# Optimization experiments

Hardware: AMD Instinct MI355X
Metric: run time of the kernel (lower is better)

The kernel has to match this reference:

```python
import jax, jax.numpy as jnp
import numpy as np

B, T, C = 4096, 64, 64

def setup_inputs() -> dict:
    key = jax.random.key(0)
    ks = jax.random.split(key, 6)
    x = jax.random.normal(ks[0], (B, T, C), dtype=jnp.float32)
    # torch Linear stores weight as [out, in]; kaiming-uniform-ish scale ~ 1/sqrt(C)
    s = 1.0 / np.sqrt(C)
    Wk = jax.random.uniform(ks[1], (C, C), jnp.float32, -s, s)
    Wq = jax.random.uniform(ks[2], (C, C), jnp.float32, -s, s)
    Wv = jax.random.uniform(ks[3], (C, C), jnp.float32, -s, s)
    Wp = jax.random.uniform(ks[4], (C, C), jnp.float32, -s, s)
    bp = jax.random.uniform(ks[5], (C,), jnp.float32, -s, s)
    return {"x": x, "Wk": Wk, "Wq": Wq, "Wv": Wv, "Wp": Wp, "bp": bp}

def reference(x, Wk, Wq, Wv, Wp, bp):
    Bc, Tc, Cc = x.shape
    k = x @ Wk.T                      # [B,T,C]
    q = x @ Wq.T
    v = x @ Wv.T
    wei = jnp.einsum('btc,bsc->bts', q, k) * (Cc ** -0.5)  # [B,T,T]
    causal = jnp.tril(jnp.ones((Tc, Tc), dtype=bool))
    wei = jnp.where(causal, wei, -jnp.inf)
    wei = jax.nn.softmax(wei, axis=-1)
    out = jnp.einsum('bts,bsc->btc', wei, v)  # [B,T,C]
    return out @ Wp.T + bp
```

## Files before the change

### kernel.cpp

```cpp
#include <hip/hip_runtime.h>
#include <hip/hip_bf16.h>


typedef __attribute__((ext_vector_type(8))) short bf16x8;
typedef __attribute__((ext_vector_type(4))) short bf16x4;
typedef __attribute__((ext_vector_type(4))) float f32x4;

#define MFMA32(a, b, c) __builtin_amdgcn_mfma_f32_16x16x32_bf16(a, b, c, 0, 0, 0)
#define LOG2E 1.44269504088896f
#define BSTR 68

__device__ __forceinline__ unsigned short f2b(float f) {
    return __builtin_bit_cast(unsigned short, __float2bfloat16(f));
}

__device__ __forceinline__ bf16x4 pack4(f32x4 a, float s) {
    bf16x4 r;
    r[0] = (short)f2b(a[0] * s); r[1] = (short)f2b(a[1] * s);
    r[2] = (short)f2b(a[2] * s); r[3] = (short)f2b(a[3] * s);
    return r;
}

__device__ __forceinline__ bf16x4 zero4() {
    bf16x4 r; r[0] = 0; r[1] = 0; r[2] = 0; r[3] = 0; return r;
}

__device__ __forceinline__ bf16x8 cat(bf16x4 lo, bf16x4 hi) {
    bf16x8 r;
    r[0] = lo[0]; r[1] = lo[1]; r[2] = lo[2]; r[3] = lo[3];
    r[4] = hi[0]; r[5] = hi[1]; r[6] = hi[2]; r[7] = hi[3];
    return r;
}

__device__ __forceinline__ bf16x8 cvt8(float4 a, float4 b) {
    bf16x8 r;
    r[0] = (short)f2b(a.x); r[1] = (short)f2b(a.y);
    r[2] = (short)f2b(a.z); r[3] = (short)f2b(a.w);
    r[4] = (short)f2b(b.x); r[5] = (short)f2b(b.y);
    r[6] = (short)f2b(b.z); r[7] = (short)f2b(b.w);
    return r;
}

__device__ __forceinline__ bf16x8 cvt8s(float4 a, float4 b, float s) {
    bf16x8 r;
    r[0] = (short)f2b(a.x * s); r[1] = (short)f2b(a.y * s);
    r[2] = (short)f2b(a.z * s); r[3] = (short)f2b(a.w * s);
    r[4] = (short)f2b(b.x * s); r[5] = (short)f2b(b.y * s);
    r[6] = (short)f2b(b.z * s); r[7] = (short)f2b(b.w * s);
    return r;
}

__device__ __forceinline__ int swz(int row, int col) {
    return row * 64 + (col ^ ((row & 7) << 3));
}

__device__ __forceinline__ void compute_batch(
    const short* __restrict__ lw, float* __restrict__ bnc, const bf16x8 xf[8],
    const float* __restrict__ bp, float* __restrict__ ob, int lane, int r, int g)
{
    const short* Wk = lw;
    const short* Wq = lw + 4096;
    const short* Wv = lw + 8192;
    const short* Wp = lw + 12288;

    bf16x8 kT8[2][4];
    #pragma unroll
    for (int cm2 = 0; cm2 < 2; ++cm2) {
        bf16x4 lo[4];
        #pragma unroll
        for (int h = 0; h < 2; ++h) {
            const int cm = cm2 * 2 + h;
            bf16x8 a0 = *(const bf16x8*)(Wk + swz(cm * 16 + r, g * 8));
            bf16x8 a1 = *(const bf16x8*)(Wk + swz(cm * 16 + r, 32 + g * 8));
            #pragma unroll
            for (int sm = 0; sm < 4; ++sm) {
                f32x4 acc = {0.f, 0.f, 0.f, 0.f};
                acc = MFMA32(a0, xf[sm * 2], acc);
                acc = MFMA32(a1, xf[sm * 2 + 1], acc);
                if (h == 0) lo[sm] = pack4(acc, 1.0f);
                else kT8[cm2][sm] = cat(lo[sm], pack4(acc, 1.0f));
            }
        }
    }

    bf16x8 q8[2][4];
    #pragma unroll
    for (int cm2 = 0; cm2 < 2; ++cm2) {
        bf16x4 lo[4];
        #pragma unroll
        for (int h = 0; h < 2; ++h) {
            const int cm = cm2 * 2 + h;
            bf16x8 a0 = *(const bf16x8*)(Wq + swz(cm * 16 + r, g * 8));
            bf16x8 a1 = *(const bf16x8*)(Wq + swz(cm * 16 + r, 32 + g * 8));
            #pragma unroll
            for (int tt = 0; tt < 4; ++tt) {
                f32x4 acc = {0.f, 0.f, 0.f, 0.f};
                acc = MFMA32(a0, xf[tt * 2], acc);
                acc = MFMA32(a1, xf[tt * 2 + 1], acc);
                if (h == 0) lo[tt] = pack4(acc, 1.0f);
                else q8[cm2][tt] = cat(lo[tt], pack4(acc, 1.0f));
            }
        }
    }

    bf16x4 P[4][4];
    #pragma unroll
    for (int tn = 0; tn < 4; ++tn) {
        f32x4 st[4];
        #pragma unroll
        for (int sm = 0; sm < 4; ++sm) {
            if (sm > tn) continue;
            f32x4 acc = {0.f, 0.f, 0.f, 0.f};
            acc = MFMA32(kT8[0][sm], q8[0][tn], acc);
            acc = MFMA32(kT8[1][sm], q8[1][tn], acc);
            st[sm] = acc;
        }
        float mx = -1e30f;
        #pragma unroll
        for (int sm = 0; sm < 4; ++sm) {
            if (sm > tn) continue;
            #pragma unroll
            for (int j = 0; j < 4; ++j) {
                float v = st[sm][j];
                if (sm == tn) v = ((g * 4 + j) <= r) ? v : -1e30f;
                st[sm][j] = v;
                mx = fmaxf(mx, v);
            }
        }
        mx = fmaxf(mx, __shfl_xor(mx, 16));
        mx = fmaxf(mx, __shfl_xor(mx, 32));
        float sum = 0.f;
        #pragma unroll
        for (int sm = 0; sm < 4; ++sm) {
            if (sm > tn) continue;
            #pragma unroll
            for (int j = 0; j < 4; ++j) {
                float e = exp2f((st[sm][j] - mx) * LOG2E);
                st[sm][j] = e;
                sum += e;
            }
        }
        sum += __shfl_xor(sum, 16);
        sum += __shfl_xor(sum, 32);
        float inv = __builtin_amdgcn_rcpf(sum);
        #pragma unroll
        for (int sm = 0; sm < 4; ++sm)
            P[sm][tn] = (sm <= tn) ? pack4(st[sm], inv) : zero4();
    }

    bf16x8 v8[4][2];
    #pragma unroll
    for (int cm = 0; cm < 4; ++cm) {
        bf16x8 b0 = *(const bf16x8*)(Wv + swz(cm * 16 + r, g * 8));
        bf16x8 b1 = *(const bf16x8*)(Wv + swz(cm * 16 + r, 32 + g * 8));
        bf16x4 tmp[4];
        #pragma unroll
        for (int tv = 0; tv < 4; ++tv) {
            f32x4 acc = {0.f, 0.f, 0.f, 0.f};
            acc = MFMA32(xf[tv * 2], b0, acc);
            acc = MFMA32(xf[tv * 2 + 1], b1, acc);
            tmp[tv] = pack4(acc, 1.0f);
        }
        v8[cm][0] = cat(tmp[0], tmp[1]);
        v8[cm][1] = cat(tmp[2], tmp[3]);
    }

    bf16x8 o28[4][2];
    #pragma unroll
    for (int tn = 0; tn < 4; ++tn) {
        bf16x8 pt80 = cat(P[0][tn], P[1][tn]);
        bf16x8 pt81 = cat(P[2][tn], P[3][tn]);
        bf16x4 c[4];
        #pragma unroll
        for (int cm = 0; cm < 4; ++cm) {
            f32x4 acc = {0.f, 0.f, 0.f, 0.f};
            acc = MFMA32(v8[cm][0], pt80, acc);
            if (tn >= 2) acc = MFMA32(v8[cm][1], pt81, acc);
            c[cm] = pack4(acc, 1.0f);
        }
        o28[tn][0] = cat(c[0], c[1]);
        o28[tn][1] = cat(c[2], c[3]);
    }

    bf16x8 wp0[4], wp1[4];
    float4 bias4[4];
    #pragma unroll
    for (int om = 0; om < 4; ++om) {
        wp0[om] = cat(*(const bf16x4*)(Wp + swz(om * 16 + r, g * 4)),
                      *(const bf16x4*)(Wp + swz(om * 16 + r, 16 + g * 4)));
        wp1[om] = cat(*(const bf16x4*)(Wp + swz(om * 16 + r, 32 + g * 4)),
                      *(const bf16x4*)(Wp + swz(om * 16 + r, 48 + g * 4)));
        bias4[om] = *(const float4*)(bp + om * 16 + g * 4);
    }
    #pragma unroll
    for (int tn = 0; tn < 4; ++tn) {
        #pragma unroll
        for (int om = 0; om < 4; ++om) {
            f32x4 acc = {0.f, 0.f, 0.f, 0.f};
            acc = MFMA32(wp0[om], o28[tn][0], acc);
            acc = MFMA32(wp1[om], o28[tn][1], acc);
            float4 o;
            o.x = acc[0] + bias4[om].x; o.y = acc[1] + bias4[om].y;
            o.z = acc[2] + bias4[om].z; o.w = acc[3] + bias4[om].w;
            *(float4*)(bnc + r * BSTR + om * 16 + g * 4) = o;
        }
        asm volatile("s_waitcnt lgkmcnt(0)" ::: "memory");
        #pragma unroll
        for (int i = 0; i < 4; ++i) {
            float4 v = *(const float4*)(bnc + (i * 4 + (lane >> 4)) * BSTR + (lane & 15) * 4);
            *(float4*)(ob + tn * 1024 + i * 256 + lane * 4) = v;
        }
        asm volatile("" ::: "memory");
    }
}

__global__ __launch_bounds__(512, 2) void attn_fused_kernel(
    const float* __restrict__ x,
    const float* __restrict__ wk,
    const float* __restrict__ wq,
    const float* __restrict__ wvw,
    const float* __restrict__ wp,
    const float* __restrict__ bp,
    float* __restrict__ out)
{
    __shared__ short lw[16384];
    __shared__ float lbounce[8 * 16 * BSTR];

    const int tid  = threadIdx.x;
    const int wv_  = tid >> 6;
    const int lane = tid & 63;
    const int r = lane & 15;
    const int g = lane >> 4;
    float* bnc = lbounce + wv_ * (16 * BSTR);
    const long b0 = (long)blockIdx.x * 8 + wv_;
    const long b1 = b0 + 2048;

    const float* xb0 = x + b0 * 4096;
    float4 raw[8][2];
    #pragma unroll
    for (int f = 0; f < 8; ++f) {
        const float* p = xb0 + ((f >> 1) * 16 + r) * 64 + (f & 1) * 32 + g * 8;
        raw[f][0] = *(const float4*)p;
        raw[f][1] = *(const float4*)(p + 4);
    }

    {
        const int row  = tid >> 1;
        const int half = tid & 1;
        const float* wsrc = (row < 64) ? wk : (row < 128) ? wq : (row < 192) ? wvw : wp;
        const float s = (row >= 64 && row < 128) ? 0.125f : 1.0f;
        const int lrow = row & 63;
        #pragma unroll
        for (int i = 0; i < 4; ++i) {
            const int grp = half * 4 + i;
            const float* p = wsrc + lrow * 64 + grp * 8;
            float4 a = *(const float4*)p;
            float4 b = *(const float4*)(p + 4);
            *(bf16x8*)(lw + row * 64 + ((grp ^ (row & 7)) * 8)) = cvt8s(a, b, s);
        }
    }

    bf16x8 xf[8];
    #pragma unroll
    for (int f = 0; f < 8; ++f)
        xf[f] = cvt8(raw[f][0], raw[f][1]);

    __syncthreads();

    const float* xb1 = x + b1 * 4096;
    float4 raw1[8][2];
    #pragma unroll
    for (int f = 0; f < 8; ++f) {
        const float* p = xb1 + ((f >> 1) * 16 + r) * 64 + (f & 1) * 32 + g * 8;
        raw1[f][0] = *(const float4*)p;
        raw1[f][1] = *(const float4*)(p + 4);
    }

    compute_batch(lw, bnc, xf, bp, out + b0 * 4096, lane, r, g);

    bf16x8 xf1[8];
    #pragma unroll
    for (int f = 0; f < 8; ++f)
        xf1[f] = cvt8(raw1[f][0], raw1[f][1]);

    compute_batch(lw, bnc, xf1, bp, out + b1 * 4096, lane, r, g);
}

extern "C" void kernel_launch(void* const* d_in, const int* in_sizes, int n_in,
                              void* d_out, int out_size, void* d_ws, size_t ws_size,
                              hipStream_t stream) {
    const float* x  = (const float*)d_in[0];
    const float* wk = (const float*)d_in[1];
    const float* wq = (const float*)d_in[2];
    const float* wv = (const float*)d_in[3];
    const float* wp = (const float*)d_in[4];
    const float* bp = (const float*)d_in[5];

    attn_fused_kernel<<<256, 512, 0, stream>>>(x, wk, wq, wv, wp, bp, (float*)d_out);
}
```

Measured before the change: 29.96 us.

## Split each batch's query tiles across a wave pair and double the grid

Each batch is now handled by two waves instead of one. One wave computes query tiles {1,2} and the other {0,3}, which balances the causal work between them. The grid doubles to 512 blocks so each CU holds more resident waves and can hide more latency. In exchange, both waves of a pair recompute the full K and V projections and load the same x rows. Each block also redoes the weight-to-LDS conversion, so total arithmetic and memory traffic grow.

```diff
diff --git a/kernel.cpp b/kernel.cpp
--- a/kernel.cpp
+++ b/kernel.cpp
@@ -54,7 +54,8 @@
     return row * 64 + (col ^ ((row & 7) << 3));
 }
 
-__device__ __forceinline__ void compute_batch(
+template<int TNA, int TNB>
+__device__ __forceinline__ void compute_half(
     const short* __restrict__ lw, float* __restrict__ bnc, const bf16x8 xf[8],
     const float* __restrict__ bp, float* __restrict__ ob, int lane, int r, int g)
 {
@@ -83,36 +84,38 @@
         }
     }
 
-    bf16x8 q8[2][4];
+    bf16x8 q8[2][2];
     #pragma unroll
     for (int cm2 = 0; cm2 < 2; ++cm2) {
-        bf16x4 lo[4];
+        bf16x4 lo[2];
         #pragma unroll
         for (int h = 0; h < 2; ++h) {
             const int cm = cm2 * 2 + h;
             bf16x8 a0 = *(const bf16x8*)(Wq + swz(cm * 16 + r, g * 8));
             bf16x8 a1 = *(const bf16x8*)(Wq + swz(cm * 16 + r, 32 + g * 8));
             #pragma unroll
-            for (int tt = 0; tt < 4; ++tt) {
+            for (int ti = 0; ti < 2; ++ti) {
+                const int tt = ti ? TNB : TNA;
                 f32x4 acc = {0.f, 0.f, 0.f, 0.f};
                 acc = MFMA32(a0, xf[tt * 2], acc);
                 acc = MFMA32(a1, xf[tt * 2 + 1], acc);
-                if (h == 0) lo[tt] = pack4(acc, 1.0f);
-                else q8[cm2][tt] = cat(lo[tt], pack4(acc, 1.0f));
+                if (h == 0) lo[ti] = pack4(acc, 1.0f);
+                else q8[cm2][ti] = cat(lo[ti], pack4(acc, 1.0f));
             }
         }
     }
 
-    bf16x4 P[4][4];
-    #pragma unroll
-    for (int tn = 0; tn < 4; ++tn) {
+    bf16x4 P[4][2];
+    #pragma unroll
+    for (int ti = 0; ti < 2; ++ti) {
+        const int tn = ti ? TNB : TNA;
         f32x4 st[4];
         #pragma unroll
         for (int sm = 0; sm < 4; ++sm) {
             if (sm > tn) continue;
             f32x4 acc = {0.f, 0.f, 0.f, 0.f};
-            acc = MFMA32(kT8[0][sm], q8[0][tn], acc);
-            acc = MFMA32(kT8[1][sm], q8[1][tn], acc);
+            acc = MFMA32(kT8[0][sm], q8[0][ti], acc);
+            acc = MFMA32(kT8[1][sm], q8[1][ti], acc);
             st[sm] = acc;
         }
         float mx = -1e30f;
@@ -145,7 +148,7 @@
         float inv = __builtin_amdgcn_rcpf(sum);
         #pragma unroll
         for (int sm = 0; sm < 4; ++sm)
-            P[sm][tn] = (sm <= tn) ? pack4(st[sm], inv) : zero4();
+            P[sm][ti] = (sm <= tn) ? pack4(st[sm], inv) : zero4();
     }
 
     bf16x8 v8[4][2];
@@ -165,11 +168,12 @@
         v8[cm][1] = cat(tmp[2], tmp[3]);
     }
 
-    bf16x8 o28[4][2];
-    #pragma unroll
-    for (int tn = 0; tn < 4; ++tn) {
-        bf16x8 pt80 = cat(P[0][tn], P[1][tn]);
-        bf16x8 pt81 = cat(P[2][tn], P[3][tn]);
+    bf16x8 o28[2][2];
+    #pragma unroll
+    for (int ti = 0; ti < 2; ++ti) {
+        const int tn = ti ? TNB : TNA;
+        bf16x8 pt80 = cat(P[0][ti], P[1][ti]);
+        bf16x8 pt81 = cat(P[2][ti], P[3][ti]);
         bf16x4 c[4];
         #pragma unroll
         for (int cm = 0; cm < 4; ++cm) {
@@ -178,8 +182,8 @@
             if (tn >= 2) acc = MFMA32(v8[cm][1], pt81, acc);
             c[cm] = pack4(acc, 1.0f);
         }
-        o28[tn][0] = cat(c[0], c[1]);
-        o28[tn][1] = cat(c[2], c[3]);
+        o28[ti][0] = cat(c[0], c[1]);
+        o28[ti][1] = cat(c[2], c[3]);
     }
 
     bf16x8 wp0[4], wp1[4];
@@ -193,12 +197,13 @@
         bias4[om] = *(const float4*)(bp + om * 16 + g * 4);
     }
     #pragma unroll
-    for (int tn = 0; tn < 4; ++tn) {
+    for (int ti = 0; ti < 2; ++ti) {
+        const int tn = ti ? TNB : TNA;
         #pragma unroll
         for (int om = 0; om < 4; ++om) {
             f32x4 acc = {0.f, 0.f, 0.f, 0.f};
-            acc = MFMA32(wp0[om], o28[tn][0], acc);
-            acc = MFMA32(wp1[om], o28[tn][1], acc);
+            acc = MFMA32(wp0[om], o28[ti][0], acc);
+            acc = MFMA32(wp1[om], o28[ti][1], acc);
             float4 o;
             o.x = acc[0] + bias4[om].x; o.y = acc[1] + bias4[om].y;
             o.z = acc[2] + bias4[om].z; o.w = acc[3] + bias4[om].w;
@@ -231,8 +236,10 @@
     const int lane = tid & 63;
     const int r = lane & 15;
     const int g = lane >> 4;
+    const int pair = wv_ >> 1;
+    const int hh   = wv_ & 1;
     float* bnc = lbounce + wv_ * (16 * BSTR);
-    const long b0 = (long)blockIdx.x * 8 + wv_;
+    const long b0 = (long)blockIdx.x * 4 + pair;
     const long b1 = b0 + 2048;
 
     const float* xb0 = x + b0 * 4096;
@@ -276,14 +283,16 @@
         raw1[f][1] = *(const float4*)(p + 4);
     }
 
-    compute_batch(lw, bnc, xf, bp, out + b0 * 4096, lane, r, g);
+    if (hh == 0) compute_half<1, 2>(lw, bnc, xf, bp, out + b0 * 4096, lane, r, g);
+    else         compute_half<0, 3>(lw, bnc, xf, bp, out + b0 * 4096, lane, r, g);
 
     bf16x8 xf1[8];
     #pragma unroll
     for (int f = 0; f < 8; ++f)
         xf1[f] = cvt8(raw1[f][0], raw1[f][1]);
 
-    compute_batch(lw, bnc, xf1, bp, out + b1 * 4096, lane, r, g);
+    if (hh == 0) compute_half<1, 2>(lw, bnc, xf1, bp, out + b1 * 4096, lane, r, g);
+    else         compute_half<0, 3>(lw, bnc, xf1, bp, out + b1 * 4096, lane, r, g);
 }
 
 extern "C" void kernel_launch(void* const* d_in, const int* in_sizes, int n_in,
@@ -296,5 +305,5 @@
     const float* wp = (const float*)d_in[4];
     const float* bp = (const float*)d_in[5];
 
-    attn_fused_kernel<<<256, 512, 0, stream>>>(x, wk, wq, wv, wp, bp, (float*)d_out);
-}
+    attn_fused_kernel<<<512, 512, 0, stream>>>(x, wk, wq, wv, wp, bp, (float*)d_out);
+}
```

Measured after the change: 37.65 us. +25.7%, slower.
